# Kernel optimization log

Measured on AMD Instinct MI355X. Metric: run time of the kernel, lower is better.

Reference implementation:

```python
import jax, jax.numpy as jnp
import numpy as np

N = 100000
E = 1600000
D_IN, D_HID, D_OUT = 128, 32, 32
NEG_SLOPE = 0.2
EPS = 1e-16


def setup_inputs() -> dict:
    key = jax.random.key(0)
    ks = jax.random.split(key, 9)
    x = jax.random.normal(ks[0], (N, D_IN), dtype=jnp.float32)
    edge_index = jax.random.randint(ks[1], (2, E), 0, N, dtype=jnp.int64)
    W1 = jax.random.normal(ks[2], (D_IN, D_HID), dtype=jnp.float32) / np.sqrt(D_IN)
    b1 = jnp.zeros((D_HID,), dtype=jnp.float32)
    W2 = jax.random.normal(ks[3], (D_HID, D_OUT), dtype=jnp.float32) / np.sqrt(D_HID)
    att_src = jax.random.normal(ks[4], (D_OUT,), dtype=jnp.float32) / np.sqrt(D_OUT)
    att_dst = jax.random.normal(ks[5], (D_OUT,), dtype=jnp.float32) / np.sqrt(D_OUT)
    b2 = jnp.zeros((D_OUT,), dtype=jnp.float32)
    return {"x": x, "edge_index": edge_index, "W1": W1, "b1": b1,
            "W2": W2, "att_src": att_src, "att_dst": att_dst, "b2": b2}


def _add_self_loops(edge_index, n):
    loop = jnp.arange(n, dtype=edge_index.dtype)
    src = jnp.concatenate([edge_index[0], loop])
    dst = jnp.concatenate([edge_index[1], loop])
    return src, dst


def _gcn_conv(x, src, dst, W, b, n):
    # symmetric normalization with self-loops already included
    deg = jax.ops.segment_sum(jnp.ones_like(dst, dtype=x.dtype), dst, num_segments=n)
    dis = jnp.where(deg > 0, jax.lax.rsqrt(jnp.maximum(deg, 1.0)), 0.0)
    h = x @ W                               # [N, H]
    norm = dis[src] * dis[dst]              # [E2]
    msg = norm[:, None] * h[src]            # [E2, H]
    return jax.ops.segment_sum(msg, dst, num_segments=n) + b


def _gat_conv(x, src, dst, W, att_src, att_dst, b, n):
    g = x @ W                               # [N, H]
    a_s = g @ att_src                       # [N]
    a_d = g @ att_dst                       # [N]
    e = a_s[src] + a_d[dst]                 # [E2]
    e = jnp.where(e > 0, e, NEG_SLOPE * e)  # leaky_relu(0.2)
    # segment softmax over edges grouped by destination node
    emax = jax.ops.segment_max(e, dst, num_segments=n)
    ee = jnp.exp(e - emax[dst])
    esum = jax.ops.segment_sum(ee, dst, num_segments=n)
    alpha = ee / (esum[dst] + EPS)
    msg = alpha[:, None] * g[src]           # [E2, H]
    return jax.ops.segment_sum(msg, dst, num_segments=n) + b


def reference(x, edge_index, W1, b1, W2, att_src, att_dst, b2):
    n = x.shape[0]
    src, dst = _add_self_loops(edge_index, n)
    h = _gcn_conv(x, src, dst, W1, b1, n)
    h = jax.nn.relu(h)
    out = _gat_conv(h, src, dst, W2, att_src, att_dst, b2, n)
    return out
```

## Files before the change

### kernel.cpp

```cpp
#include <hip/hip_runtime.h>
#include <cstdint>
#include <cstddef>

#define D_IN   128
#define D_HID  32
#define D_OUT  32
#define NEG_SLOPE 0.2f
#define EPS_F  1e-16f

#define BKT_SHIFT 9
#define NPB (1 << BKT_SHIFT)
#define KBUKMAX 256
#define NBLK_BIN 512
#define AGG_BLOCKS 2048

using half4 = __attribute__((ext_vector_type(4))) _Float16;

__global__ void detect_kernel(const int* __restrict__ ei, long long E, int* __restrict__ flag) {
    const int t = threadIdx.x;
    long long n = E < 64 ? E : 64;
    int bad = (t < n && ei[2 * t + 1] != 0) ? 1 : 0;
    unsigned long long mask = __ballot(bad);
    if (t == 0) *flag = (mask == 0ULL) ? 1 : 0;
}

__device__ __forceinline__ int edge_val(const int* __restrict__ ei, long long idx, int is64) {
    return is64 ? ei[idx * 2] : ei[idx];
}

__global__ __launch_bounds__(256) void hist_kernel(
        const int* __restrict__ ei, const int* __restrict__ flag,
        long long E, long long E2, int* __restrict__ hist, int K2, int EPB) {
    __shared__ int hcnt[KBUKMAX];
    const int is64 = *flag;
    const int t = threadIdx.x;
    if (t < K2) hcnt[t] = 0;
    __syncthreads();
    const long long lo = (long long)blockIdx.x * EPB;
    const long long hi = min(E2, lo + EPB);
    for (long long e = lo + t; e < hi; e += 256) {
        int d = (e < E) ? edge_val(ei, E + e, is64) : (int)(e - E);
        atomicAdd(&hcnt[d >> BKT_SHIFT], 1);
    }
    __syncthreads();
    if (t < K2) hist[t * gridDim.x + blockIdx.x] = hcnt[t];
}

__global__ void scan_ga_kernel(int* __restrict__ a, int* __restrict__ bsum, int L) {
    __shared__ int wsum[4];
    const int t = threadIdx.x;
    const int i0 = blockIdx.x * 1024 + t * 4;
    int v[4]; int s = 0;
    #pragma unroll
    for (int k = 0; k < 4; ++k) {
        v[k] = (i0 + k < L) ? a[i0 + k] : 0;
        s += v[k];
    }
    const int lane = t & 63, wid = t >> 6;
    int incl = s;
    #pragma unroll
    for (int d = 1; d < 64; d <<= 1) {
        int u = __shfl_up(incl, d);
        if (lane >= d) incl += u;
    }
    if (lane == 63) wsum[wid] = incl;
    __syncthreads();
    int woff = 0;
    for (int w = 0; w < wid; ++w) woff += wsum[w];
    int excl = woff + incl - s;
    #pragma unroll
    for (int k = 0; k < 4; ++k) {
        if (i0 + k < L) a[i0 + k] = excl;
        excl += v[k];
    }
    if (t == 255) bsum[blockIdx.x] = woff + incl;
}

__global__ __launch_bounds__(1024) void scan_flat_kernel(int* __restrict__ a, int L) {
    __shared__ int wsum[16];
    __shared__ int carry_s;
    const int t = threadIdx.x;
    const int lane = t & 63, wid = t >> 6;
    if (t == 0) carry_s = 0;
    __syncthreads();
    for (int start = 0; start < L; start += 1024) {
        int idx = start + t;
        int v = (idx < L) ? a[idx] : 0;
        int incl = v;
        #pragma unroll
        for (int d = 1; d < 64; d <<= 1) {
            int u = __shfl_up(incl, d);
            if (lane >= d) incl += u;
        }
        if (lane == 63) wsum[wid] = incl;
        __syncthreads();
        int woff = 0;
        for (int w = 0; w < wid; ++w) woff += wsum[w];
        int carry = carry_s;
        __syncthreads();
        if (idx < L) a[idx] = carry + woff + incl - v;
        if (t == 1023) carry_s = carry + woff + incl;
        __syncthreads();
    }
}

__global__ void scan_gc_kernel(int* __restrict__ a, const int* __restrict__ bsum, int L) {
    int idx = blockIdx.x * blockDim.x + threadIdx.x;
    if (idx < L) a[idx] += bsum[idx >> 10];
}

__global__ __launch_bounds__(256) void scatter_kernel(
        const int* __restrict__ ei, const int* __restrict__ flag,
        long long E, long long E2, const int* __restrict__ off,
        unsigned* __restrict__ bins, int K2, int EPB) {
    __shared__ int cur[KBUKMAX];
    const int is64 = *flag;
    const int t = threadIdx.x;
    if (t < K2) cur[t] = off[t * gridDim.x + blockIdx.x];
    __syncthreads();
    const long long lo = (long long)blockIdx.x * EPB;
    const long long hi = min(E2, lo + EPB);
    for (long long e = lo + t; e < hi; e += 256) {
        int s, d;
        if (e < E) { s = edge_val(ei, e, is64); d = edge_val(ei, E + e, is64); }
        else       { s = d = (int)(e - E); }
        int b = d >> BKT_SHIFT;
        int pos = atomicAdd(&cur[b], 1);
        bins[pos] = (unsigned)s | ((unsigned)(d & (NPB - 1)) << 17);
    }
}

__global__ __launch_bounds__(512) void csr_b_kernel(
        const unsigned* __restrict__ bins, const int* __restrict__ off,
        int* __restrict__ rowptr, float* __restrict__ dis, int* __restrict__ csr_src,
        int N, int K2, long long E2) {
    __shared__ int lcur[NPB];
    __shared__ int wsum[8];
    const int b = blockIdx.x, t = threadIdx.x;
    const int nbase = b << BKT_SHIFT;
    const int nn = min(NPB, N - nbase);
    lcur[t] = 0;
    __syncthreads();
    const int base = off[b * NBLK_BIN];
    const int end  = (b == K2 - 1) ? (int)E2 : off[(b + 1) * NBLK_BIN];
    for (int i = base + t; i < end; i += 512)
        atomicAdd(&lcur[bins[i] >> 17], 1);
    __syncthreads();
    const int lane = t & 63, wid = t >> 6;
    int v = lcur[t];
    int incl = v;
    #pragma unroll
    for (int d = 1; d < 64; d <<= 1) {
        int u = __shfl_up(incl, d);
        if (lane >= d) incl += u;
    }
    if (lane == 63) wsum[wid] = incl;
    __syncthreads();
    int woff = 0;
    for (int w = 0; w < wid; ++w) woff += wsum[w];
    int excl = woff + incl - v;
    if (t < nn) {
        rowptr[nbase + t] = base + excl;
        dis[nbase + t] = rsqrtf((float)v);
    }
    __syncthreads();
    lcur[t] = base + excl;
    __syncthreads();
    for (int i = base + t; i < end; i += 512) {
        unsigned u = bins[i];
        int pos = atomicAdd(&lcur[u >> 17], 1);
        csr_src[pos] = (int)(u & 0x1FFFFu);
    }
    if (b == 0 && t == 0) rowptr[N] = (int)E2;
}

__global__ __launch_bounds__(256) void gemm1_kernel(
        const float* __restrict__ x, const float* __restrict__ W1,
        const float* __restrict__ dis, _Float16* __restrict__ hws_h, int N) {
    __shared__ float sWt[D_HID][D_IN + 4];
    const int t = threadIdx.x;
    for (int i = t; i < D_IN * D_HID; i += 256) {
        int k = i >> 5, c = i & 31;
        sWt[c][k] = W1[i];
    }
    __syncthreads();
    const int c_t = t & 7;
    const int r_t = t >> 3;
    const long long row0 = (long long)blockIdx.x * 128 + (long long)r_t * 4;
    const float4* x4 = (const float4*)x;
    float acc[4][4];
    #pragma unroll
    for (int i = 0; i < 4; ++i)
        #pragma unroll
        for (int j = 0; j < 4; ++j) acc[i][j] = 0.f;
    long long r[4]; bool val[4];
    #pragma unroll
    for (int i = 0; i < 4; ++i) {
        long long rr = row0 + i;
        val[i] = rr < N;
        r[i] = val[i] ? rr : (long long)(N - 1);
    }
    #pragma unroll 4
    for (int q = 0; q < 32; ++q) {
        float4 wv[4];
        #pragma unroll
        for (int j = 0; j < 4; ++j)
            wv[j] = *(const float4*)&sWt[c_t * 4 + j][q * 4];
        #pragma unroll
        for (int i = 0; i < 4; ++i) {
            float4 xv = x4[r[i] * 32 + q];
            #pragma unroll
            for (int j = 0; j < 4; ++j) {
                acc[i][j] = fmaf(xv.x, wv[j].x, acc[i][j]);
                acc[i][j] = fmaf(xv.y, wv[j].y, acc[i][j]);
                acc[i][j] = fmaf(xv.z, wv[j].z, acc[i][j]);
                acc[i][j] = fmaf(xv.w, wv[j].w, acc[i][j]);
            }
        }
    }
    half4* hh4 = (half4*)hws_h;
    #pragma unroll
    for (int i = 0; i < 4; ++i) {
        if (val[i]) {
            float dd = dis[r[i]];
            half4 o;
            o.x = (_Float16)(acc[i][0] * dd); o.y = (_Float16)(acc[i][1] * dd);
            o.z = (_Float16)(acc[i][2] * dd); o.w = (_Float16)(acc[i][3] * dd);
            hh4[r[i] * 8 + c_t] = o;
        }
    }
}

__global__ void gcn_agg_kernel(const int* __restrict__ rowptr, const int* __restrict__ csr_src,
                               const _Float16* __restrict__ hws_h, const float* __restrict__ dis,
                               const float* __restrict__ b1, float* __restrict__ h1, int N) {
    const int lane = threadIdx.x & 63;
    const int u = lane & 7, grp = lane >> 3;
    const int wib = threadIdx.x >> 6;
    const half4* hh4 = (const half4*)hws_h;
    float4* h14 = (float4*)h1;
    const float4 b14 = ((const float4*)b1)[u];
    for (int i = blockIdx.x * 4 + wib; i < N; i += gridDim.x * 4) {
        const int b = rowptr[i], e = rowptr[i + 1];
        float ax = 0.f, ay = 0.f, az = 0.f, aw = 0.f;
        for (int j = b + grp; j < e; j += 8) {
            int s = csr_src[j];
            half4 hv = hh4[s * 8 + u];
            ax += (float)hv.x; ay += (float)hv.y;
            az += (float)hv.z; aw += (float)hv.w;
        }
        #pragma unroll
        for (int d = 8; d <= 32; d <<= 1) {
            ax += __shfl_xor(ax, d); ay += __shfl_xor(ay, d);
            az += __shfl_xor(az, d); aw += __shfl_xor(aw, d);
        }
        if (grp == 0) {
            float dd = dis[i];
            float4 o;
            o.x = fmaf(dd, ax, b14.x); o.y = fmaf(dd, ay, b14.y);
            o.z = fmaf(dd, az, b14.z); o.w = fmaf(dd, aw, b14.w);
            o.x = o.x > 0.f ? o.x : 0.f; o.y = o.y > 0.f ? o.y : 0.f;
            o.z = o.z > 0.f ? o.z : 0.f; o.w = o.w > 0.f ? o.w : 0.f;
            h14[(long long)i * 8 + u] = o;
        }
    }
}

__global__ void gemm2_kernel(const float* __restrict__ h1, const float* __restrict__ W2,
                             const float* __restrict__ att_s, const float* __restrict__ att_d,
                             _Float16* __restrict__ g_h, float* __restrict__ a_s,
                             float* __restrict__ a_d, int N) {
    __shared__ float sW[D_HID * D_OUT];
    __shared__ float sas[D_OUT], sad[D_OUT];
    __shared__ float sh[8][D_HID];
    const int t = threadIdx.x;
    const int c = t & 31, r = t >> 5;
    for (int i = t; i < D_HID * D_OUT; i += 256) sW[i] = W2[i];
    if (t < D_OUT) { sas[t] = att_s[t]; sad[t] = att_d[t]; }
    for (long long base = (long long)blockIdx.x * 8; base < N; base += (long long)gridDim.x * 8) {
        __syncthreads();
        if (base * D_HID + t < (long long)N * D_HID) sh[r][c] = h1[base * D_HID + t];
        __syncthreads();
        long long row = base + r;
        if (row < N) {
            float gv = 0.0f;
            #pragma unroll
            for (int k = 0; k < D_HID; ++k) gv = fmaf(sh[r][k], sW[k * D_OUT + c], gv);
            g_h[row * D_OUT + c] = (_Float16)gv;
            float ps = gv * sas[c];
            float pd = gv * sad[c];
            #pragma unroll
            for (int d = 16; d >= 1; d >>= 1) {
                ps += __shfl_xor(ps, d);
                pd += __shfl_xor(pd, d);
            }
            if (c == 0) { a_s[row] = ps; a_d[row] = pd; }
        }
    }
}

__global__ __launch_bounds__(256) void e_pre_kernel(
        const int* __restrict__ rowptr, const int* __restrict__ csr_src,
        const float* __restrict__ a_s, const float* __restrict__ a_d,
        float* __restrict__ epre, int N) {
    int i = blockIdx.x * blockDim.x + threadIdx.x;
    if (i >= N) return;
    const int b = rowptr[i], e = rowptr[i + 1];
    const float adi = a_d[i];
    for (int j = b; j < e; ++j) {
        float ev = a_s[csr_src[j]] + adi;
        epre[j] = ev > 0.f ? ev : NEG_SLOPE * ev;
    }
}

__global__ void gat_agg_kernel(const int* __restrict__ rowptr, const int* __restrict__ csr_src,
                               const _Float16* __restrict__ g_h, const float* __restrict__ epre,
                               const float* __restrict__ b2, float* __restrict__ out, int N) {
    const int lane = threadIdx.x & 63;
    const int u = lane & 7, grp = lane >> 3;
    const int wib = threadIdx.x >> 6;
    const half4* gh4 = (const half4*)g_h;
    float4* out4 = (float4*)out;
    const float4 b24 = ((const float4*)b2)[u];
    for (int i = blockIdx.x * 4 + wib; i < N; i += gridDim.x * 4) {
        const int b = rowptr[i], e = rowptr[i + 1];
        float m = -1e30f, ssum = 0.f;
        float ax = 0.f, ay = 0.f, az = 0.f, aw = 0.f;
        for (int j = b + grp; j < e; j += 8) {
            int s = csr_src[j];
            float ev = epre[j];
            float mn = fmaxf(m, ev);
            float scale = __expf(m - mn);
            float w = __expf(ev - mn);
            half4 gv = gh4[s * 8 + u];
            ssum = ssum * scale + w;
            ax = fmaf(ax, scale, w * (float)gv.x);
            ay = fmaf(ay, scale, w * (float)gv.y);
            az = fmaf(az, scale, w * (float)gv.z);
            aw = fmaf(aw, scale, w * (float)gv.w);
            m = mn;
        }
        #pragma unroll
        for (int d = 8; d <= 32; d <<= 1) {
            float mo = __shfl_xor(m, d);
            float so = __shfl_xor(ssum, d);
            float ox = __shfl_xor(ax, d), oy = __shfl_xor(ay, d);
            float oz = __shfl_xor(az, d), ow = __shfl_xor(aw, d);
            float M = fmaxf(m, mo);
            float e0 = __expf(m - M), e1 = __expf(mo - M);
            ssum = ssum * e0 + so * e1;
            ax = ax * e0 + ox * e1; ay = ay * e0 + oy * e1;
            az = az * e0 + oz * e1; aw = aw * e0 + ow * e1;
            m = M;
        }
        if (grp == 0) {
            float inv = 1.f / (ssum + EPS_F);
            float4 o;
            o.x = fmaf(ax, inv, b24.x); o.y = fmaf(ay, inv, b24.y);
            o.z = fmaf(az, inv, b24.z); o.w = fmaf(aw, inv, b24.w);
            out4[(long long)i * 8 + u] = o;
        }
    }
}

extern "C" void kernel_launch(void* const* d_in, const int* in_sizes, int n_in,
                              void* d_out, int out_size, void* d_ws, size_t ws_size,
                              hipStream_t stream) {
    const float* x       = (const float*)d_in[0];
    const int*   ei      = (const int*)d_in[1];
    const float* W1      = (const float*)d_in[2];
    const float* b1      = (const float*)d_in[3];
    const float* W2      = (const float*)d_in[4];
    const float* att_src = (const float*)d_in[5];
    const float* att_dst = (const float*)d_in[6];
    const float* b2      = (const float*)d_in[7];
    float* out = (float*)d_out;

    const long long N  = in_sizes[0] / D_IN;
    const long long E  = in_sizes[1] / 2;
    const long long E2 = E + N;
    const int K2  = (int)((N + NPB - 1) >> BKT_SHIFT);
    const int EPB = (int)((E2 + NBLK_BIN - 1) / NBLK_BIN);
    const int LH  = K2 * NBLK_BIN;
    const int NBH = (LH + 1023) / 1024;

    char* ws = (char*)d_ws;
    size_t off0 = 0;
    auto alloc = [&](size_t bytes) -> void* {
        off0 = (off0 + 255) & ~(size_t)255;
        void* p = ws + off0;
        off0 += bytes;
        return p;
    };
    int*   flag     = (int*)  alloc(16);
    int*   hist     = (int*)  alloc((size_t)KBUKMAX * NBLK_BIN * 4);
    unsigned* bins  = (unsigned*)alloc((size_t)E2 * 4);
    int*   rowptr   = (int*)  alloc((size_t)(N + 1) * 4);
    int*   csr_src  = (int*)  alloc((size_t)E2 * 4);
    float* dis      = (float*)alloc((size_t)N * 4);
    _Float16* hws_h = (_Float16*)alloc((size_t)N * D_HID * 2);
    float* h1       = (float*)alloc((size_t)N * D_HID * 4);
    _Float16* g_h   = (_Float16*)alloc((size_t)N * D_OUT * 2);
    float* as       = (float*)alloc((size_t)N * 4);
    float* ad       = (float*)alloc((size_t)N * 4);
    float* epre     = (float*)alloc((size_t)E2 * 4);
    int*   bsum     = (int*)  alloc((size_t)NBH * 4);
    (void)ws_size; (void)n_in; (void)out_size;

    detect_kernel<<<1, 64, 0, stream>>>(ei, E, flag);
    hist_kernel<<<NBLK_BIN, 256, 0, stream>>>(ei, flag, E, E2, hist, K2, EPB);
    scan_ga_kernel<<<NBH, 256, 0, stream>>>(hist, bsum, LH);
    scan_flat_kernel<<<1, 1024, 0, stream>>>(bsum, NBH);
    scan_gc_kernel<<<(LH + 255) / 256, 256, 0, stream>>>(hist, bsum, LH);
    scatter_kernel<<<NBLK_BIN, 256, 0, stream>>>(ei, flag, E, E2, hist, bins, K2, EPB);
    csr_b_kernel<<<K2, 512, 0, stream>>>(bins, hist, rowptr, dis, csr_src, (int)N, K2, E2);
    gemm1_kernel<<<(int)((N + 127) / 128), 256, 0, stream>>>(x, W1, dis, hws_h, (int)N);
    gcn_agg_kernel<<<AGG_BLOCKS, 256, 0, stream>>>(rowptr, csr_src, hws_h, dis, b1, h1, (int)N);
    gemm2_kernel<<<1024, 256, 0, stream>>>(h1, W2, att_src, att_dst, g_h, as, ad, (int)N);
    e_pre_kernel<<<(int)((N + 255) / 256), 256, 0, stream>>>(rowptr, csr_src, as, ad, epre, (int)N);
    gat_agg_kernel<<<AGG_BLOCKS, 256, 0, stream>>>(rowptr, csr_src, g_h, epre, b2, out, (int)N);
}
```

Before: 191.6 us.

## Precompute softmax weights per node, unroll aggregation loops, drop shared-memory W1 in gemm1

The edge pre-pass now computes the per-destination max and the exponentiated weights, and stores a per-node inverse sum. This removes the online-softmax rescaling and the exp-heavy shuffle merge from the GAT aggregation, which becomes a plain weighted sum. Both aggregation loops process two edges per iteration to keep more gathers in flight. gemm1 reads W1 directly from global/cache instead of shared memory, with 2 rows per thread and twice the blocks. The trade-off is a serial per-thread double pass over each node's edges in e_pre, with an extra read and write of the weight array.

```diff
diff --git a/kernel.cpp b/kernel.cpp
--- a/kernel.cpp
+++ b/kernel.cpp
@@ -177,50 +177,46 @@
 __global__ __launch_bounds__(256) void gemm1_kernel(
         const float* __restrict__ x, const float* __restrict__ W1,
         const float* __restrict__ dis, _Float16* __restrict__ hws_h, int N) {
-    __shared__ float sWt[D_HID][D_IN + 4];
-    const int t = threadIdx.x;
-    for (int i = t; i < D_IN * D_HID; i += 256) {
-        int k = i >> 5, c = i & 31;
-        sWt[c][k] = W1[i];
-    }
-    __syncthreads();
+    const int t = threadIdx.x;
     const int c_t = t & 7;
     const int r_t = t >> 3;
-    const long long row0 = (long long)blockIdx.x * 128 + (long long)r_t * 4;
+    const long long row0 = (long long)blockIdx.x * 64 + (long long)r_t * 2;
     const float4* x4 = (const float4*)x;
-    float acc[4][4];
-    #pragma unroll
-    for (int i = 0; i < 4; ++i)
+    const float4* W4 = (const float4*)W1;
+    float acc[2][4];
+    #pragma unroll
+    for (int i = 0; i < 2; ++i)
         #pragma unroll
         for (int j = 0; j < 4; ++j) acc[i][j] = 0.f;
-    long long r[4]; bool val[4];
-    #pragma unroll
-    for (int i = 0; i < 4; ++i) {
+    long long r[2]; bool val[2];
+    #pragma unroll
+    for (int i = 0; i < 2; ++i) {
         long long rr = row0 + i;
         val[i] = rr < N;
         r[i] = val[i] ? rr : (long long)(N - 1);
     }
     #pragma unroll 4
     for (int q = 0; q < 32; ++q) {
-        float4 wv[4];
+        float4 xv0 = x4[r[0] * 32 + q];
+        float4 xv1 = x4[r[1] * 32 + q];
         #pragma unroll
-        for (int j = 0; j < 4; ++j)
-            wv[j] = *(const float4*)&sWt[c_t * 4 + j][q * 4];
-        #pragma unroll
-        for (int i = 0; i < 4; ++i) {
-            float4 xv = x4[r[i] * 32 + q];
-            #pragma unroll
-            for (int j = 0; j < 4; ++j) {
-                acc[i][j] = fmaf(xv.x, wv[j].x, acc[i][j]);
-                acc[i][j] = fmaf(xv.y, wv[j].y, acc[i][j]);
-                acc[i][j] = fmaf(xv.z, wv[j].z, acc[i][j]);
-                acc[i][j] = fmaf(xv.w, wv[j].w, acc[i][j]);
-            }
+        for (int kk = 0; kk < 4; ++kk) {
+            float4 wv = W4[(q * 4 + kk) * 8 + c_t];
+            float xs0 = (&xv0.x)[kk];
+            float xs1 = (&xv1.x)[kk];
+            acc[0][0] = fmaf(xs0, wv.x, acc[0][0]);
+            acc[0][1] = fmaf(xs0, wv.y, acc[0][1]);
+            acc[0][2] = fmaf(xs0, wv.z, acc[0][2]);
+            acc[0][3] = fmaf(xs0, wv.w, acc[0][3]);
+            acc[1][0] = fmaf(xs1, wv.x, acc[1][0]);
+            acc[1][1] = fmaf(xs1, wv.y, acc[1][1]);
+            acc[1][2] = fmaf(xs1, wv.z, acc[1][2]);
+            acc[1][3] = fmaf(xs1, wv.w, acc[1][3]);
         }
     }
     half4* hh4 = (half4*)hws_h;
     #pragma unroll
-    for (int i = 0; i < 4; ++i) {
+    for (int i = 0; i < 2; ++i) {
         if (val[i]) {
             float dd = dis[r[i]];
             half4 o;
@@ -243,11 +239,18 @@
     for (int i = blockIdx.x * 4 + wib; i < N; i += gridDim.x * 4) {
         const int b = rowptr[i], e = rowptr[i + 1];
         float ax = 0.f, ay = 0.f, az = 0.f, aw = 0.f;
-        for (int j = b + grp; j < e; j += 8) {
-            int s = csr_src[j];
-            half4 hv = hh4[s * 8 + u];
-            ax += (float)hv.x; ay += (float)hv.y;
-            az += (float)hv.z; aw += (float)hv.w;
+        for (int j = b + grp; j < e; j += 16) {
+            int j1 = j + 8;
+            int s0 = csr_src[j];
+            bool v1 = j1 < e;
+            int s1 = v1 ? csr_src[j1] : s0;
+            float w1 = v1 ? 1.f : 0.f;
+            half4 h0 = hh4[s0 * 8 + u];
+            half4 h1v = hh4[s1 * 8 + u];
+            ax += (float)h0.x + w1 * (float)h1v.x;
+            ay += (float)h0.y + w1 * (float)h1v.y;
+            az += (float)h0.z + w1 * (float)h1v.z;
+            aw += (float)h0.w + w1 * (float)h1v.w;
         }
         #pragma unroll
         for (int d = 8; d <= 32; d <<= 1) {
@@ -302,20 +305,31 @@
 __global__ __launch_bounds__(256) void e_pre_kernel(
         const int* __restrict__ rowptr, const int* __restrict__ csr_src,
         const float* __restrict__ a_s, const float* __restrict__ a_d,
-        float* __restrict__ epre, int N) {
+        float* __restrict__ wexp, float* __restrict__ inv, int N) {
     int i = blockIdx.x * blockDim.x + threadIdx.x;
     if (i >= N) return;
     const int b = rowptr[i], e = rowptr[i + 1];
     const float adi = a_d[i];
+    float m = -1e30f;
     for (int j = b; j < e; ++j) {
         float ev = a_s[csr_src[j]] + adi;
-        epre[j] = ev > 0.f ? ev : NEG_SLOPE * ev;
-    }
+        ev = ev > 0.f ? ev : NEG_SLOPE * ev;
+        wexp[j] = ev;
+        m = fmaxf(m, ev);
+    }
+    float ssum = 0.f;
+    for (int j = b; j < e; ++j) {
+        float w = __expf(wexp[j] - m);
+        wexp[j] = w;
+        ssum += w;
+    }
+    inv[i] = 1.f / (ssum + EPS_F);
 }
 
 __global__ void gat_agg_kernel(const int* __restrict__ rowptr, const int* __restrict__ csr_src,
-                               const _Float16* __restrict__ g_h, const float* __restrict__ epre,
-                               const float* __restrict__ b2, float* __restrict__ out, int N) {
+                               const _Float16* __restrict__ g_h, const float* __restrict__ wexp,
+                               const float* __restrict__ inv, const float* __restrict__ b2,
+                               float* __restrict__ out, int N) {
     const int lane = threadIdx.x & 63;
     const int u = lane & 7, grp = lane >> 3;
     const int wib = threadIdx.x >> 6;
@@ -324,40 +338,31 @@
     const float4 b24 = ((const float4*)b2)[u];
     for (int i = blockIdx.x * 4 + wib; i < N; i += gridDim.x * 4) {
         const int b = rowptr[i], e = rowptr[i + 1];
-        float m = -1e30f, ssum = 0.f;
         float ax = 0.f, ay = 0.f, az = 0.f, aw = 0.f;
-        for (int j = b + grp; j < e; j += 8) {
-            int s = csr_src[j];
-            float ev = epre[j];
-            float mn = fmaxf(m, ev);
-            float scale = __expf(m - mn);
-            float w = __expf(ev - mn);
-            half4 gv = gh4[s * 8 + u];
-            ssum = ssum * scale + w;
-            ax = fmaf(ax, scale, w * (float)gv.x);
-            ay = fmaf(ay, scale, w * (float)gv.y);
-            az = fmaf(az, scale, w * (float)gv.z);
-            aw = fmaf(aw, scale, w * (float)gv.w);
-            m = mn;
+        for (int j = b + grp; j < e; j += 16) {
+            int j1 = j + 8;
+            int s0 = csr_src[j];
+            float w0 = wexp[j];
+            bool v1 = j1 < e;
+            int s1 = v1 ? csr_src[j1] : s0;
+            float w1 = v1 ? wexp[j1] : 0.f;
+            half4 g0 = gh4[s0 * 8 + u];
+            half4 g1 = gh4[s1 * 8 + u];
+            ax = fmaf(w0, (float)g0.x, fmaf(w1, (float)g1.x, ax));
+            ay = fmaf(w0, (float)g0.y, fmaf(w1, (float)g1.y, ay));
+            az = fmaf(w0, (float)g0.z, fmaf(w1, (float)g1.z, az));
+            aw = fmaf(w0, (float)g0.w, fmaf(w1, (float)g1.w, aw));
         }
         #pragma unroll
         for (int d = 8; d <= 32; d <<= 1) {
-            float mo = __shfl_xor(m, d);
-            float so = __shfl_xor(ssum, d);
-            float ox = __shfl_xor(ax, d), oy = __shfl_xor(ay, d);
-            float oz = __shfl_xor(az, d), ow = __shfl_xor(aw, d);
-            float M = fmaxf(m, mo);
-            float e0 = __expf(m - M), e1 = __expf(mo - M);
-            ssum = ssum * e0 + so * e1;
-            ax = ax * e0 + ox * e1; ay = ay * e0 + oy * e1;
-            az = az * e0 + oz * e1; aw = aw * e0 + ow * e1;
-            m = M;
+            ax += __shfl_xor(ax, d); ay += __shfl_xor(ay, d);
+            az += __shfl_xor(az, d); aw += __shfl_xor(aw, d);
         }
         if (grp == 0) {
-            float inv = 1.f / (ssum + EPS_F);
+            float iv = inv[i];
             float4 o;
-            o.x = fmaf(ax, inv, b24.x); o.y = fmaf(ay, inv, b24.y);
-            o.z = fmaf(az, inv, b24.z); o.w = fmaf(aw, inv, b24.w);
+            o.x = fmaf(ax, iv, b24.x); o.y = fmaf(ay, iv, b24.y);
+            o.z = fmaf(az, iv, b24.z); o.w = fmaf(aw, iv, b24.w);
             out4[(long long)i * 8 + u] = o;
         }
     }
@@ -403,7 +408,8 @@
     _Float16* g_h   = (_Float16*)alloc((size_t)N * D_OUT * 2);
     float* as       = (float*)alloc((size_t)N * 4);
     float* ad       = (float*)alloc((size_t)N * 4);
-    float* epre     = (float*)alloc((size_t)E2 * 4);
+    float* wexp     = (float*)alloc((size_t)E2 * 4);
+    float* inv      = (float*)alloc((size_t)N * 4);
     int*   bsum     = (int*)  alloc((size_t)NBH * 4);
     (void)ws_size; (void)n_in; (void)out_size;
 
@@ -414,9 +420,9 @@
     scan_gc_kernel<<<(LH + 255) / 256, 256, 0, stream>>>(hist, bsum, LH);
     scatter_kernel<<<NBLK_BIN, 256, 0, stream>>>(ei, flag, E, E2, hist, bins, K2, EPB);
     csr_b_kernel<<<K2, 512, 0, stream>>>(bins, hist, rowptr, dis, csr_src, (int)N, K2, E2);
-    gemm1_kernel<<<(int)((N + 127) / 128), 256, 0, stream>>>(x, W1, dis, hws_h, (int)N);
+    gemm1_kernel<<<(int)((N + 63) / 64), 256, 0, stream>>>(x, W1, dis, hws_h, (int)N);
     gcn_agg_kernel<<<AGG_BLOCKS, 256, 0, stream>>>(rowptr, csr_src, hws_h, dis, b1, h1, (int)N);
     gemm2_kernel<<<1024, 256, 0, stream>>>(h1, W2, att_src, att_dst, g_h, as, ad, (int)N);
-    e_pre_kernel<<<(int)((N + 255) / 256), 256, 0, stream>>>(rowptr, csr_src, as, ad, epre, (int)N);
-    gat_agg_kernel<<<AGG_BLOCKS, 256, 0, stream>>>(rowptr, csr_src, g_h, epre, b2, out, (int)N);
-}
+    e_pre_kernel<<<(int)((N + 255) / 256), 256, 0, stream>>>(rowptr, csr_src, as, ad, wexp, inv, (int)N);
+    gat_agg_kernel<<<AGG_BLOCKS, 256, 0, stream>>>(rowptr, csr_src, g_h, wexp, inv, b2, out, (int)N);
+}
```

New measurement: 213.1 us. +11.3%, slower.
